# Optimization experiments

Measured on AMD Instinct MI355X. Metric: run time of the kernel, lower is better.

Reference implementation:

```python
import jax, jax.numpy as jnp
import numpy as np

B, L, DN, DE, DD, H = 2, 512, 512, 128, 128, 8
DK, DEH, DDH = DN // H, DE // H, DD // H
F = 2 * DK + DEH + 2 * DDH  # per-head concat feature size (176)
SLOPE = 0.2


def _kaiming(key, out_f, in_f):
    bound = np.sqrt(6.0 / ((1.0 + SLOPE ** 2) * in_f))
    return jax.random.uniform(key, (out_f, in_f), minval=-bound, maxval=bound, dtype=jnp.float32)


def lin(x, w, b):
    y = jnp.einsum('...i,oi->...o', x, w)
    return y if b is None else y + b


def setup_inputs() -> dict:
    key = jax.random.key(0)
    ks = jax.random.split(key, 16)
    inp = {
        'node_representation': jax.random.normal(ks[0], (B, L, DN), dtype=jnp.float32),
        'edge_representation': jax.random.normal(ks[1], (B, L, L, DE), dtype=jnp.float32),
        'diff_vec': jax.random.normal(ks[2], (B, L, DD), dtype=jnp.float32),
        'Wn_w': _kaiming(ks[3], DN, DN), 'Wn_b': jnp.zeros((DN,), jnp.float32),
        'We_w': _kaiming(ks[4], DE, DE), 'We_b': jnp.zeros((DE,), jnp.float32),
        'Wd_w': _kaiming(ks[5], DD, DD), 'Wd_b': jnp.zeros((DD,), jnp.float32),
        'Wh_w': _kaiming(ks[6], DK, DK), 'Wh_b': jnp.zeros((DK,), jnp.float32),
        'attn_w': _kaiming(ks[7], 1, F),
        'outn_w': _kaiming(ks[8], DN, DN), 'outn_b': jnp.zeros((DN,), jnp.float32),
        'Wn2_w': _kaiming(ks[9], DN, DN), 'Wn2_b': jnp.zeros((DN,), jnp.float32),
        'We2_w': _kaiming(ks[10], DE, DE), 'We2_b': jnp.zeros((DE,), jnp.float32),
        'Wd2_w': _kaiming(ks[11], DD, DD), 'Wd2_b': jnp.zeros((DD,), jnp.float32),
        'edge_w': _kaiming(ks[12], DEH, F), 'edge_b': jnp.zeros((DEH,), jnp.float32),
        'oute_w': _kaiming(ks[13], DE, DE), 'oute_b': jnp.zeros((DE,), jnp.float32),
    }
    return inp


def reference(node_representation, edge_representation, diff_vec,
              Wn_w, Wn_b, We_w, We_b, Wd_w, Wd_b, Wh_w, Wh_b, attn_w,
              outn_w, outn_b, Wn2_w, Wn2_b, We2_w, We2_b, Wd2_w, Wd2_b,
              edge_w, edge_b, oute_w, oute_b):
    lrelu = lambda x: jax.nn.leaky_relu(x, SLOPE)

    # ---- node update (GAT-style with concat score decomposed per term) ----
    npj = lin(node_representation, Wn_w, Wn_b).reshape(B, L, H, DK)
    epj = lin(edge_representation, We_w, We_b).reshape(B, L, L, H, DEH)
    dpj = lin(diff_vec, Wd_w, Wd_b).reshape(B, L, H, DDH)
    a = attn_w[0]  # concat order: [hi, hj, edge, di, dj]
    a_hi, a_hj = a[:DK], a[DK:2 * DK]
    a_e = a[2 * DK:2 * DK + DEH]
    a_di, a_dj = a[2 * DK + DEH:2 * DK + DEH + DDH], a[-DDH:]
    # scores[b,i,j,h]
    s = (jnp.einsum('blhd,d->blh', npj, a_hi)[:, :, None, :]
         + jnp.einsum('blhd,d->blh', npj, a_hj)[:, None, :, :]
         + jnp.einsum('blmhe,e->blmh', epj, a_e)
         + jnp.einsum('blhd,d->blh', dpj, a_di)[:, :, None, :]
         + jnp.einsum('blhd,d->blh', dpj, a_dj)[:, None, :, :])
    diag = jnp.eye(L, dtype=bool)[None, :, :, None]
    s = jnp.where(diag, -jnp.inf, s)
    probs = jax.nn.softmax(lrelu(s), axis=2)  # softmax over j
    node_wh = lin(npj, Wh_w, Wh_b)  # [B,L,H,DK]
    agg = jnp.einsum('blmh,bmhd->blhd', probs, node_wh)
    new_node = (npj + lrelu(agg)).reshape(B, L, DN)
    new_node = lin(new_node, outn_w, outn_b)

    # ---- edge update (concat-linear decomposed into per-term matmuls) ----
    np2 = lin(new_node, Wn2_w, Wn2_b).reshape(B, L, H, DK)
    ep2 = lin(edge_representation, We2_w, We2_b).reshape(B, L, L, H, DEH)
    dp2 = lin(diff_vec, Wd2_w, Wd2_b).reshape(B, L, H, DDH)
    # edge concat order: [edge, hi, hj, di, dj]
    W_e = edge_w[:, :DEH]
    W_hi = edge_w[:, DEH:DEH + DK]
    W_hj = edge_w[:, DEH + DK:DEH + 2 * DK]
    W_di = edge_w[:, DEH + 2 * DK:DEH + 2 * DK + DDH]
    W_dj = edge_w[:, -DDH:]
    e_out = (jnp.einsum('blmhe,fe->blmhf', ep2, W_e)
             + jnp.einsum('blhd,fd->blhf', np2, W_hi)[:, :, None]
             + jnp.einsum('blhd,fd->blhf', np2, W_hj)[:, None]
             + jnp.einsum('blhd,fd->blhf', dp2, W_di)[:, :, None]
             + jnp.einsum('blhd,fd->blhf', dp2, W_dj)[:, None]
             + edge_b)
    new_edge = lin(e_out.reshape(B, L, L, DE), oute_w, oute_b)
    return new_node, new_edge
```

## Files before the change

### kernel.cpp

```cpp
#include <hip/hip_runtime.h>
#include <hip/hip_bf16.h>

typedef unsigned short u16;
typedef unsigned short u16x8 __attribute__((ext_vector_type(8)));
typedef __bf16 bf16x8 __attribute__((ext_vector_type(8)));
typedef float f32x4 __attribute__((ext_vector_type(4)));

#define LRS 0.2f

__device__ __forceinline__ u16 f2b(float f) {
  __hip_bfloat16 h = __float2bfloat16(f);
  return __builtin_bit_cast(u16, h);
}

template<int K, int O, int KSEG, int R>
__device__ __forceinline__ void gemm_rowsR(const float* xr, const float* W, const float* bias,
                                           float* yl, float* yg, int ygstride) {
  constexpr int KPT = K / KSEG;
  constexpr int OPP = 256 / KSEG;
  const int t = threadIdx.x;
  const int ks = t % KSEG;
  const int oi = t / KSEG;
#pragma unroll
  for (int pass = 0; pass < O / OPP; ++pass) {
    const int o = pass * OPP + oi;
    float a[R];
#pragma unroll
    for (int r = 0; r < R; ++r) a[r] = 0.0f;
    const float* wp = W + (size_t)o * K + ks * KPT;
    const float* xb = xr + ks * KPT;
#pragma unroll 4
    for (int kc = 0; kc < KPT; kc += 4) {
      f32x4 w4 = *(const f32x4*)(wp + kc);
#pragma unroll
      for (int r = 0; r < R; ++r) {
        f32x4 x = *(const f32x4*)(xb + r * K + kc);
#pragma unroll
        for (int j = 0; j < 4; ++j) a[r] += x[j] * w4[j];
      }
    }
#pragma unroll
    for (int d = 1; d < KSEG; d <<= 1)
#pragma unroll
      for (int r = 0; r < R; ++r) a[r] += __shfl_xor(a[r], d, 64);
    if (ks == 0) {
      float bv = bias ? bias[o] : 0.0f;
#pragma unroll
      for (int r = 0; r < R; ++r) {
        float v = a[r] + bv;
        if (yl) yl[r * O + o] = v;
        if (yg) yg[(size_t)r * ygstride + o] = v;
      }
    }
  }
}

__global__ __launch_bounds__(256) void kW1(const float* We_w, const float* We_b, const float* attn,
                                           const float* We2_w, const float* We2_b,
                                           const float* edge_w, const float* edge_b,
                                           float* Mfull, u16* vb, float* cbe, float* sconst) {
  int gid = blockIdx.x * 256 + threadIdx.x;
  if (gid < 16384) {
    int hf = gid >> 7, c = gid & 127;
    int h = hf >> 4, fo = hf & 15;
    float s = 0;
    for (int e = 0; e < 16; ++e)
      s += edge_w[fo * 176 + e] * We2_w[(h * 16 + e) * 128 + c];
    Mfull[hf * 128 + c] = s;
  } else if (gid < 16384 + 2048) {
    int idx = gid - 16384;
    int c = idx >> 4, hc = idx & 15;
    float s = 0;
    if (hc < 8)
      for (int e = 0; e < 16; ++e)
        s += We_w[(hc * 16 + e) * 128 + c] * attn[128 + e];
    vb[c * 16 + hc] = f2b(s);
  } else if (gid < 18432 + 128) {
    int hf = gid - 18432;
    int h = hf >> 4, fo = hf & 15;
    float s = edge_b[fo];
    for (int e = 0; e < 16; ++e)
      s += We2_b[h * 16 + e] * edge_w[fo * 176 + e];
    cbe[hf] = s;
  } else if (gid < 18560 + 8) {
    int h = gid - 18560;
    float s = 0;
    for (int e = 0; e < 16; ++e)
      s += We_b[h * 16 + e] * attn[128 + e];
    sconst[h] = s;
  }
}

__global__ __launch_bounds__(256) void kW2(const float* oute_w, const float* Mfull, u16* Gb) {
  int gid = blockIdx.x * 256 + threadIdx.x;
  int o = gid >> 7, c = gid & 127;
  float s = 0;
  for (int k = 0; k < 128; ++k)
    s += oute_w[o * 128 + k] * Mfull[k * 128 + c];
  Gb[o * 128 + c] = f2b(s);
}

__global__ __launch_bounds__(256) void kN1(const float* node, const float* diff,
                                           const float* Wn_w, const float* Wn_b,
                                           const float* Wd_w, const float* Wd_b,
                                           const float* Wh_w, const float* Wh_b,
                                           const float* attn, const float* sconst,
                                           float* npj_g, float* nwh_g,
                                           float* srow_g, float* scol_g) {
  __shared__ float nrow[2 * 512], npjl[2 * 512], drow[2 * 128], dpjl[2 * 128];
  const int t = threadIdx.x;
  const int r0 = blockIdx.x * 2;
  *(f32x4*)&nrow[t * 4] = *(const f32x4*)(node + (size_t)r0 * 512 + t * 4);
  if (t < 64) *(f32x4*)&drow[t * 4] = *(const f32x4*)(diff + (size_t)r0 * 128 + t * 4);
  __syncthreads();
  gemm_rowsR<512, 512, 4, 2>(nrow, Wn_w, Wn_b, npjl, npj_g + (size_t)r0 * 512, 512);
  gemm_rowsR<128, 128, 4, 2>(drow, Wd_w, Wd_b, dpjl, nullptr, 0);
  __syncthreads();
  {
    int d = t & 63, hh = t >> 6;
#pragma unroll
    for (int hi = 0; hi < 2; ++hi) {
      int h = hh + hi * 4;
      float wb = Wh_b[d];
      float acc[2] = {wb, wb};
      for (int k = 0; k < 64; ++k) {
        float w = Wh_w[d * 64 + k];
#pragma unroll
        for (int r = 0; r < 2; ++r) acc[r] += npjl[r * 512 + h * 64 + k] * w;
      }
#pragma unroll
      for (int r = 0; r < 2; ++r) nwh_g[(size_t)(r0 + r) * 512 + h * 64 + d] = acc[r];
    }
  }
  if (t < 16) {
    int r = t >> 3, h = t & 7;
    float shi = 0, shj = 0, sdi = 0, sdj = 0;
    for (int d = 0; d < 64; ++d) {
      float x = npjl[r * 512 + h * 64 + d];
      shi += x * attn[d];
      shj += x * attn[64 + d];
    }
    for (int e = 0; e < 16; ++e) {
      float x = dpjl[r * 128 + h * 16 + e];
      sdi += x * attn[144 + e];
      sdj += x * attn[160 + e];
    }
    srow_g[(r0 + r) * 8 + h] = shi + sdi + sconst[h];
    scol_g[(r0 + r) * 8 + h] = shj + sdj;
  }
}

__global__ __launch_bounds__(256) void kA(const float* edge, const float* srow, const float* scol,
                                          const u16* vb, u16* P, float* invs, u16* abf) {
  __shared__ u16 At[2][8192];
  __shared__ float smx[512 * 9];
  __shared__ float red[256];
  __shared__ float mxh8[8];
  const int bl = blockIdx.x;
  const int b = bl >> 9, l = bl & 511;
  const int t = threadIdx.x;
  const int lane = t & 63, w = t >> 6;
  const int colL = lane & 15, kg = lane >> 4;
  const int h = t & 7, seg = t >> 3;

  bf16x8 bfr[4];
#pragma unroll
  for (int ks = 0; ks < 4; ++ks) {
    u16x8 u;
#pragma unroll
    for (int j = 0; j < 8; ++j) u[j] = vb[(ks * 32 + kg * 8 + j) * 16 + colL];
    bfr[ks] = __builtin_bit_cast(bf16x8, u);
  }

  const float* eb = edge + (size_t)bl * 65536;
  f32x4 va[8], vn[8];
#pragma unroll
  for (int j = 0; j < 4; ++j) {
    va[2 * j]     = *(const f32x4*)(eb + j * 2048 + t * 8);
    va[2 * j + 1] = *(const f32x4*)(eb + j * 2048 + t * 8 + 4);
  }
  for (int tl = 0; tl < 8; ++tl) {
    u16* cdst = abf ? abf + ((size_t)bl * 8 + tl) * 8192 : nullptr;
    u16* lbuf = At[tl & 1];
#pragma unroll
    for (int j = 0; j < 4; ++j) {
      u16x8 a8;
#pragma unroll
      for (int q = 0; q < 4; ++q) { a8[q] = f2b(va[2 * j][q]); a8[4 + q] = f2b(va[2 * j + 1][q]); }
      int c = j * 256 + t;
      int row = c >> 4, cu = c & 15;
      *(u16x8*)(lbuf + (row * 16 + (cu ^ (row & 7))) * 8) = a8;
      if (cdst) *(u16x8*)(cdst + c * 8) = a8;
    }
    if (tl < 7) {
      const float* nb2 = eb + (tl + 1) * 8192;
#pragma unroll
      for (int j = 0; j < 4; ++j) {
        vn[2 * j]     = *(const f32x4*)(nb2 + j * 2048 + t * 8);
        vn[2 * j + 1] = *(const f32x4*)(nb2 + j * 2048 + t * 8 + 4);
      }
    }
    __syncthreads();
    f32x4 acc = {0, 0, 0, 0};
#pragma unroll
    for (int ks = 0; ks < 4; ++ks) {
      int cu = ks * 4 + kg;
      int lrow = w * 16 + colL;
      bf16x8 af = *(bf16x8*)(lbuf + (lrow * 16 + (cu ^ (lrow & 7))) * 8);
      acc = __builtin_amdgcn_mfma_f32_16x16x32_bf16(af, bfr[ks], acc, 0, 0, 0);
    }
    if (colL < 8) {
#pragma unroll
      for (int r = 0; r < 4; ++r)
        smx[(tl * 64 + w * 16 + kg * 4 + r) * 9 + colL] = acc[r];
    }
#pragma unroll
    for (int q = 0; q < 8; ++q) va[q] = vn[q];
  }
  __syncthreads();

  const float srh2 = srow[(size_t)bl * 8 + h];
  float mx = -__builtin_inff();
#pragma unroll 4
  for (int i = 0; i < 16; ++i) {
    int m = seg * 16 + i;
    float sv = smx[m * 9 + h] + srh2 + scol[((size_t)b * 512 + m) * 8 + h];
    sv = (m == l) ? -__builtin_inff() : (sv >= 0.0f ? sv : LRS * sv);
    smx[m * 9 + h] = sv;
    mx = fmaxf(mx, sv);
  }
  red[t] = mx;
  __syncthreads();
  if (t < 8) {
    float m2 = -__builtin_inff();
    for (int sg = 0; sg < 32; ++sg) m2 = fmaxf(m2, red[sg * 8 + t]);
    mxh8[t] = m2;
  }
  __syncthreads();
  float mh = mxh8[h];
  float smv = 0;
#pragma unroll 4
  for (int i = 0; i < 16; ++i) {
    int m = seg * 16 + i;
    float p = __expf(smx[m * 9 + h] - mh);
    smx[m * 9 + h] = p;
    smv += p;
  }
  red[t] = smv;
  __syncthreads();
  if (t < 8) {
    float s2 = 0;
    for (int sg = 0; sg < 32; ++sg) s2 += red[sg * 8 + t];
    invs[(size_t)bl * 8 + t] = 1.0f / s2;
  }
  __syncthreads();
#pragma unroll
  for (int k = 0; k < 2; ++k) {
    int c = k * 256 + t;
    int hp = c >> 6, mb = (c & 63) * 8;
    u16x8 pk;
#pragma unroll
    for (int j = 0; j < 8; ++j) pk[j] = f2b(smx[(mb + j) * 9 + hp]);
    *(u16x8*)(P + (((size_t)b * 8 + hp) * 512 + l) * 512 + mb) = pk;
  }
}

__global__ __launch_bounds__(256) void kAgg(const u16* P, const float* nwh, const float* npj,
                                            const float* invs, float* nnp) {
  __shared__ u16 Pt[8192];
  __shared__ u16 Vt[8192];
  const int bid = blockIdx.x;
  const int lt = bid & 7, h = (bid >> 3) & 7, b = bid >> 6;
  const int l0 = lt * 64;
  const int t = threadIdx.x;
  const int lane = t & 63, w = t >> 6;
  const int colL = lane & 15, kg = lane >> 4;

  f32x4 acc[4] = {};
  for (int mc = 0; mc < 4; ++mc) {
#pragma unroll
    for (int q = 0; q < 4; ++q) {
      int c = q * 256 + t;
      int row = c >> 4, cu = c & 15;
      u16x8 a8 = *(const u16x8*)(P + (((size_t)b * 8 + h) * 512 + l0 + row) * 512 + mc * 128 + cu * 8);
      *(u16x8*)(Pt + (row * 16 + (cu ^ (row & 7))) * 8) = a8;
    }
#pragma unroll
    for (int q = 0; q < 8; ++q) {
      int c = q * 256 + t;
      int m = c >> 4, d4 = (c & 15) * 4;
      f32x4 v = *(const f32x4*)(nwh + ((size_t)b * 512 + mc * 128 + m) * 512 + h * 64 + d4);
#pragma unroll
      for (int j = 0; j < 4; ++j) {
        int d = d4 + j;
        Vt[(d * 16 + ((m >> 3) ^ (d & 7))) * 8 + (m & 7)] = f2b(v[j]);
      }
    }
    __syncthreads();
#pragma unroll
    for (int kc = 0; kc < 4; ++kc) {
      int cu = kc * 4 + kg;
      int prow = w * 16 + colL;
      bf16x8 af = *(bf16x8*)(Pt + (prow * 16 + (cu ^ (prow & 7))) * 8);
#pragma unroll
      for (int n = 0; n < 4; ++n) {
        int d = n * 16 + colL;
        bf16x8 bf = *(bf16x8*)(Vt + (d * 16 + (cu ^ (d & 7))) * 8);
        acc[n] = __builtin_amdgcn_mfma_f32_16x16x32_bf16(af, bf, acc[n], 0, 0, 0);
      }
    }
    __syncthreads();
  }
#pragma unroll
  for (int r = 0; r < 4; ++r) {
    int l = l0 + w * 16 + kg * 4 + r;
    float iv = invs[((size_t)b * 512 + l) * 8 + h];
#pragma unroll
    for (int n = 0; n < 4; ++n) {
      int o = h * 64 + n * 16 + colL;
      size_t idx = ((size_t)b * 512 + l) * 512 + o;
      float a = acc[n][r] * iv;
      a = a >= 0.0f ? a : LRS * a;
      nnp[idx] = npj[idx] + a;
    }
  }
}

__global__ __launch_bounds__(256) void kN234(const float* nnp, const float* diff,
                                             const float* outn_w, const float* outn_b,
                                             const float* Wn2_w, const float* Wn2_b,
                                             const float* Wd2_w, const float* Wd2_b,
                                             const float* edge_w, const float* cbe,
                                             const float* oute_w, const float* oute_b,
                                             float* out0, float* Pl, float* Pm) {
  __shared__ float xr[2 * 512], o0l[2 * 512], np2l[2 * 512], dr[2 * 128], dp2l[2 * 128];
  __shared__ float Rls[2 * 128], Rms[2 * 128];
  const int t = threadIdx.x;
  const int r0 = blockIdx.x * 2;
  *(f32x4*)&xr[t * 4] = *(const f32x4*)(nnp + (size_t)r0 * 512 + t * 4);
  if (t < 64) *(f32x4*)&dr[t * 4] = *(const f32x4*)(diff + (size_t)r0 * 128 + t * 4);
  __syncthreads();
  gemm_rowsR<512, 512, 4, 2>(xr, outn_w, outn_b, o0l, out0 + (size_t)r0 * 512, 512);
  gemm_rowsR<128, 128, 4, 2>(dr, Wd2_w, Wd2_b, dp2l, nullptr, 0);
  __syncthreads();
  gemm_rowsR<512, 512, 4, 2>(o0l, Wn2_w, Wn2_b, np2l, nullptr, 0);
  __syncthreads();
  {
    int hf = t & 127, which = t >> 7;
    int h = hf >> 4, fo = hf & 15;
    const float* wh = edge_w + fo * 176 + 16 + which * 64;
    const float* wd = edge_w + fo * 176 + 144 + which * 16;
    float add = which ? 0.0f : cbe[hf];
    float* dst = which ? Rms : Rls;
#pragma unroll
    for (int r = 0; r < 2; ++r) {
      float a = add;
      for (int d = 0; d < 64; ++d) a += np2l[r * 512 + h * 64 + d] * wh[d];
      for (int e = 0; e < 16; ++e) a += dp2l[r * 128 + h * 16 + e] * wd[e];
      dst[r * 128 + hf] = a;
    }
  }
  __syncthreads();
  gemm_rowsR<128, 128, 4, 2>(Rls, oute_w, oute_b, nullptr, Pl + (size_t)r0 * 128, 128);
  gemm_rowsR<128, 128, 4, 2>(Rms, oute_w, nullptr, nullptr, Pm + (size_t)r0 * 128, 128);
}

__global__ __launch_bounds__(256) void kEc(const u16* Abf, const u16* Gb,
                                           const float* Pl, const float* Pm, float* oute) {
  __shared__ u16 Gt[16384];
  __shared__ u16 At[8192];
  const int tile = blockIdx.x;
  const int bl = tile >> 2;
  const int b = bl >> 9;
  const int q0 = (tile & 3) * 128;
  const int t = threadIdx.x, lane = t & 63, w = t >> 6;
#pragma unroll
  for (int i2 = 0; i2 < 8; ++i2) {
    int u = i2 * 256 + t;
    int row = u >> 4, cu = u & 15;
    *(u16x8*)(Gt + (row * 16 + (cu ^ (row & 7))) * 8) = *(const u16x8*)(Gb + u * 8);
  }
  const int wr = w >> 1, wc = w & 1;
  const int colL = lane & 15, kg = lane >> 4;
  const float* plp = Pl + (size_t)bl * 128;
  f32x4 plv4[4];
#pragma unroll
  for (int n = 0; n < 4; ++n) plv4[n] = *(const f32x4*)(plp + wc * 64 + n * 16 + kg * 4);

  for (int sub = 0; sub < 2; ++sub) {
    const int r0 = q0 + sub * 64;
    const int gs = (tile & 3) * 2 + sub;
    const u16* src = Abf + ((size_t)bl * 8 + gs) * 8192;
#pragma unroll
    for (int q = 0; q < 4; ++q) {
      int c = q * 256 + t;
      u16x8 a8 = *(const u16x8*)(src + c * 8);
      int row = c >> 4, cu = c & 15;
      *(u16x8*)(At + (row * 16 + (cu ^ (row & 7))) * 8) = a8;
    }
    __syncthreads();
    f32x4 acc[2][4] = {};
#pragma unroll
    for (int ks = 0; ks < 4; ++ks) {
      int cu = ks * 4 + kg;
      bf16x8 af[2], bfv[4];
#pragma unroll
      for (int i = 0; i < 2; ++i) {
        int row = wr * 32 + i * 16 + colL;
        af[i] = *(bf16x8*)(At + (row * 16 + (cu ^ (row & 7))) * 8);
      }
#pragma unroll
      for (int n = 0; n < 4; ++n) {
        int orow = wc * 64 + n * 16 + colL;
        bfv[n] = *(bf16x8*)(Gt + (orow * 16 + (cu ^ (orow & 7))) * 8);
      }
#pragma unroll
      for (int i = 0; i < 2; ++i)
#pragma unroll
        for (int n = 0; n < 4; ++n)
          acc[i][n] = __builtin_amdgcn_mfma_f32_16x16x32_bf16(bfv[n], af[i], acc[i][n], 0, 0, 0);
    }
    float* ob = oute + ((size_t)bl * 512 + r0) * 128;
#pragma unroll
    for (int i = 0; i < 2; ++i) {
      int m = wr * 32 + i * 16 + colL;
      const float* pmp = Pm + ((size_t)b * 512 + r0 + m) * 128;
      float* orow = ob + (size_t)m * 128;
#pragma unroll
      for (int n = 0; n < 4; ++n) {
        int oc = wc * 64 + n * 16 + kg * 4;
        f32x4 pm4 = *(const f32x4*)(pmp + oc);
        f32x4 o4;
#pragma unroll
        for (int r = 0; r < 4; ++r) o4[r] = acc[i][n][r] + plv4[n][r] + pm4[r];
        *(f32x4*)(orow + oc) = o4;
      }
    }
    __syncthreads();
  }
}

__global__ __launch_bounds__(256) void kEd(const float* edge, const u16* Gb,
                                           const float* Pl, const float* Pm, float* oute) {
  __shared__ u16 Gt[16384];
  __shared__ u16 At[8192];
  const int tile = blockIdx.x;
  const int bl = tile >> 2;
  const int b = bl >> 9;
  const int q0 = (tile & 3) * 128;
  const int t = threadIdx.x, lane = t & 63, w = t >> 6;
#pragma unroll
  for (int i2 = 0; i2 < 8; ++i2) {
    int u = i2 * 256 + t;
    int row = u >> 4, cu = u & 15;
    *(u16x8*)(Gt + (row * 16 + (cu ^ (row & 7))) * 8) = *(const u16x8*)(Gb + u * 8);
  }
  const int wr = w >> 1, wc = w & 1;
  const int colL = lane & 15, kg = lane >> 4;
  const float* plp = Pl + (size_t)bl * 128;
  f32x4 plv4[4];
#pragma unroll
  for (int n = 0; n < 4; ++n) plv4[n] = *(const f32x4*)(plp + wc * 64 + n * 16 + kg * 4);
  const int arow = t >> 2, aseg = t & 3;

  for (int sub = 0; sub < 2; ++sub) {
    const int r0 = q0 + sub * 64;
    {
      const float* p = edge + ((size_t)bl * 512 + r0 + arow) * 128 + aseg * 32;
      f32x4 v[8];
#pragma unroll
      for (int q = 0; q < 8; ++q) v[q] = *(const f32x4*)(p + q * 4);
#pragma unroll
      for (int jj = 0; jj < 4; ++jj) {
        u16x8 a8;
#pragma unroll
        for (int j2 = 0; j2 < 4; ++j2) {
          a8[j2]     = f2b(v[2 * jj][j2]);
          a8[4 + j2] = f2b(v[2 * jj + 1][j2]);
        }
        int cu = aseg * 4 + jj;
        *(u16x8*)(At + (arow * 16 + (cu ^ (arow & 7))) * 8) = a8;
      }
    }
    __syncthreads();
    f32x4 acc[2][4] = {};
#pragma unroll
    for (int ks = 0; ks < 4; ++ks) {
      int cu = ks * 4 + kg;
      bf16x8 af[2], bfv[4];
#pragma unroll
      for (int i = 0; i < 2; ++i) {
        int row = wr * 32 + i * 16 + colL;
        af[i] = *(bf16x8*)(At + (row * 16 + (cu ^ (row & 7))) * 8);
      }
#pragma unroll
      for (int n = 0; n < 4; ++n) {
        int orow = wc * 64 + n * 16 + colL;
        bfv[n] = *(bf16x8*)(Gt + (orow * 16 + (cu ^ (orow & 7))) * 8);
      }
#pragma unroll
      for (int i = 0; i < 2; ++i)
#pragma unroll
        for (int n = 0; n < 4; ++n)
          acc[i][n] = __builtin_amdgcn_mfma_f32_16x16x32_bf16(bfv[n], af[i], acc[i][n], 0, 0, 0);
    }
    float* ob = oute + ((size_t)bl * 512 + r0) * 128;
#pragma unroll
    for (int i = 0; i < 2; ++i) {
      int m = wr * 32 + i * 16 + colL;
      const float* pmp = Pm + ((size_t)b * 512 + r0 + m) * 128;
      float* orow = ob + (size_t)m * 128;
#pragma unroll
      for (int n = 0; n < 4; ++n) {
        int oc = wc * 64 + n * 16 + kg * 4;
        f32x4 pm4 = *(const f32x4*)(pmp + oc);
        f32x4 o4;
#pragma unroll
        for (int r = 0; r < 4; ++r) o4[r] = acc[i][n][r] + plv4[n][r] + pm4[r];
        *(f32x4*)(orow + oc) = o4;
      }
    }
    __syncthreads();
  }
}

extern "C" void kernel_launch(void* const* d_in, const int* in_sizes, int n_in,
                              void* d_out, int out_size, void* d_ws, size_t ws_size,
                              hipStream_t stream) {
  (void)in_sizes; (void)n_in; (void)out_size;
  const float* node   = (const float*)d_in[0];
  const float* edge   = (const float*)d_in[1];
  const float* diff   = (const float*)d_in[2];
  const float* Wn_w   = (const float*)d_in[3];
  const float* Wn_b   = (const float*)d_in[4];
  const float* We_w   = (const float*)d_in[5];
  const float* We_b   = (const float*)d_in[6];
  const float* Wd_w   = (const float*)d_in[7];
  const float* Wd_b   = (const float*)d_in[8];
  const float* Wh_w   = (const float*)d_in[9];
  const float* Wh_b   = (const float*)d_in[10];
  const float* attn   = (const float*)d_in[11];
  const float* outn_w = (const float*)d_in[12];
  const float* outn_b = (const float*)d_in[13];
  const float* Wn2_w  = (const float*)d_in[14];
  const float* Wn2_b  = (const float*)d_in[15];
  const float* We2_w  = (const float*)d_in[16];
  const float* We2_b  = (const float*)d_in[17];
  const float* Wd2_w  = (const float*)d_in[18];
  const float* Wd2_b  = (const float*)d_in[19];
  const float* edge_w = (const float*)d_in[20];
  const float* edge_b = (const float*)d_in[21];
  const float* oute_w = (const float*)d_in[22];
  const float* oute_b = (const float*)d_in[23];

  float* out0 = (float*)d_out;
  float* out1 = out0 + 524288;

  float* f = (float*)d_ws;
  size_t off = 0;
  auto alloc = [&](size_t n) { float* p = f + off; off += (n + 7) & ~(size_t)7; return p; };
  float* npj    = alloc(524288);
  float* nwh    = alloc(524288);
  float* srow   = alloc(8192);
  float* scol   = alloc(8192);
  float* sconst = alloc(8);
  float* cbe    = alloc(128);
  float* Mfull  = alloc(16384);
  float* nnp    = alloc(524288);
  float* Pl     = alloc(131072);
  float* Pm     = alloc(131072);
  float* invs   = alloc(8192);
  u16* vb = (u16*)(f + off); off += 1024;
  u16* Gb = (u16*)(f + off); off += 8192;
  u16* P  = (u16*)(f + off); off += 2097152;
  const size_t abf_elems = (size_t)2 * 512 * 512 * 128;
  bool cache = ws_size >= off * 4 + abf_elems * 2 + 256;
  u16* Abf = cache ? (u16*)(f + off) : nullptr;

  hipLaunchKernelGGL(kW1, dim3(73), dim3(256), 0, stream,
                     We_w, We_b, attn, We2_w, We2_b, edge_w, edge_b, Mfull, vb, cbe, sconst);
  hipLaunchKernelGGL(kW2, dim3(64), dim3(256), 0, stream, oute_w, Mfull, Gb);
  hipLaunchKernelGGL(kN1, dim3(512), dim3(256), 0, stream,
                     node, diff, Wn_w, Wn_b, Wd_w, Wd_b, Wh_w, Wh_b, attn, sconst,
                     npj, nwh, srow, scol);
  hipLaunchKernelGGL(kA, dim3(1024), dim3(256), 0, stream,
                     edge, srow, scol, vb, P, invs, Abf);
  hipLaunchKernelGGL(kAgg, dim3(128), dim3(256), 0, stream, P, nwh, npj, invs, nnp);
  hipLaunchKernelGGL(kN234, dim3(512), dim3(256), 0, stream,
                     nnp, diff, outn_w, outn_b, Wn2_w, Wn2_b, Wd2_w, Wd2_b,
                     edge_w, cbe, oute_w, oute_b, out0, Pl, Pm);
  if (cache)
    hipLaunchKernelGGL(kEc, dim3(4096), dim3(256), 0, stream, Abf, Gb, Pl, Pm, out1);
  else
    hipLaunchKernelGGL(kEd, dim3(4096), dim3(256), 0, stream, edge, Gb, Pl, Pm, out1);
}
```

Measured before the change: 460.1 us.

## Feed MFMA from registers in kA and shrink edge-output tiles with register-held weights

kA no longer stages each edge tile through a double-buffered LDS array with block barriers. Each wave now loads its own rows from global memory, converts them to bf16 and passes them straight to MFMA, while still writing the cached bf16 copy in row-major order. kEc/kEd now handle 64 rows per block over twice as many blocks, with each wave keeping its slice of the G weight in registers instead of copying the whole matrix to LDS. This removes barriers and LDS traffic and frees LDS for occupancy, at the cost of less latency hiding in kA, which no longer prefetches, and redundant G loads per block.

```diff
diff --git a/kernel.cpp b/kernel.cpp
--- a/kernel.cpp
+++ b/kernel.cpp
@@ -152,7 +152,6 @@
 
 __global__ __launch_bounds__(256) void kA(const float* edge, const float* srow, const float* scol,
                                           const u16* vb, u16* P, float* invs, u16* abf) {
-  __shared__ u16 At[2][8192];
   __shared__ float smx[512 * 9];
   __shared__ float red[256];
   __shared__ float mxh8[8];
@@ -173,49 +172,28 @@
   }
 
   const float* eb = edge + (size_t)bl * 65536;
-  f32x4 va[8], vn[8];
-#pragma unroll
-  for (int j = 0; j < 4; ++j) {
-    va[2 * j]     = *(const f32x4*)(eb + j * 2048 + t * 8);
-    va[2 * j + 1] = *(const f32x4*)(eb + j * 2048 + t * 8 + 4);
-  }
-  for (int tl = 0; tl < 8; ++tl) {
-    u16* cdst = abf ? abf + ((size_t)bl * 8 + tl) * 8192 : nullptr;
-    u16* lbuf = At[tl & 1];
-#pragma unroll
-    for (int j = 0; j < 4; ++j) {
+  u16* cb = abf ? abf + (size_t)bl * 65536 : nullptr;
+
+  for (int ci = 0; ci < 8; ++ci) {
+    const int r0 = w * 128 + ci * 16;
+    const int row = r0 + colL;
+    const float* rp = eb + (size_t)row * 128;
+    f32x4 acc = {0, 0, 0, 0};
+#pragma unroll
+    for (int ks = 0; ks < 4; ++ks) {
+      f32x4 e0 = *(const f32x4*)(rp + ks * 32 + kg * 8);
+      f32x4 e1 = *(const f32x4*)(rp + ks * 32 + kg * 8 + 4);
       u16x8 a8;
 #pragma unroll
-      for (int q = 0; q < 4; ++q) { a8[q] = f2b(va[2 * j][q]); a8[4 + q] = f2b(va[2 * j + 1][q]); }
-      int c = j * 256 + t;
-      int row = c >> 4, cu = c & 15;
-      *(u16x8*)(lbuf + (row * 16 + (cu ^ (row & 7))) * 8) = a8;
-      if (cdst) *(u16x8*)(cdst + c * 8) = a8;
-    }
-    if (tl < 7) {
-      const float* nb2 = eb + (tl + 1) * 8192;
-#pragma unroll
-      for (int j = 0; j < 4; ++j) {
-        vn[2 * j]     = *(const f32x4*)(nb2 + j * 2048 + t * 8);
-        vn[2 * j + 1] = *(const f32x4*)(nb2 + j * 2048 + t * 8 + 4);
-      }
-    }
-    __syncthreads();
-    f32x4 acc = {0, 0, 0, 0};
-#pragma unroll
-    for (int ks = 0; ks < 4; ++ks) {
-      int cu = ks * 4 + kg;
-      int lrow = w * 16 + colL;
-      bf16x8 af = *(bf16x8*)(lbuf + (lrow * 16 + (cu ^ (lrow & 7))) * 8);
-      acc = __builtin_amdgcn_mfma_f32_16x16x32_bf16(af, bfr[ks], acc, 0, 0, 0);
+      for (int j = 0; j < 4; ++j) { a8[j] = f2b(e0[j]); a8[4 + j] = f2b(e1[j]); }
+      if (cb) *(u16x8*)(cb + (size_t)row * 128 + ks * 32 + kg * 8) = a8;
+      acc = __builtin_amdgcn_mfma_f32_16x16x32_bf16(__builtin_bit_cast(bf16x8, a8), bfr[ks], acc, 0, 0, 0);
     }
     if (colL < 8) {
 #pragma unroll
       for (int r = 0; r < 4; ++r)
-        smx[(tl * 64 + w * 16 + kg * 4 + r) * 9 + colL] = acc[r];
-    }
-#pragma unroll
-    for (int q = 0; q < 8; ++q) va[q] = vn[q];
+        smx[(r0 + kg * 4 + r) * 9 + colL] = acc[r];
+    }
   }
   __syncthreads();
 
@@ -367,160 +345,136 @@
 
 __global__ __launch_bounds__(256) void kEc(const u16* Abf, const u16* Gb,
                                            const float* Pl, const float* Pm, float* oute) {
-  __shared__ u16 Gt[16384];
   __shared__ u16 At[8192];
   const int tile = blockIdx.x;
-  const int bl = tile >> 2;
+  const int bl = tile >> 3;
   const int b = bl >> 9;
-  const int q0 = (tile & 3) * 128;
+  const int r0 = (tile & 7) * 64;
   const int t = threadIdx.x, lane = t & 63, w = t >> 6;
-#pragma unroll
-  for (int i2 = 0; i2 < 8; ++i2) {
-    int u = i2 * 256 + t;
-    int row = u >> 4, cu = u & 15;
-    *(u16x8*)(Gt + (row * 16 + (cu ^ (row & 7))) * 8) = *(const u16x8*)(Gb + u * 8);
-  }
-  const int wr = w >> 1, wc = w & 1;
   const int colL = lane & 15, kg = lane >> 4;
-  const float* plp = Pl + (size_t)bl * 128;
-  f32x4 plv4[4];
-#pragma unroll
-  for (int n = 0; n < 4; ++n) plv4[n] = *(const f32x4*)(plp + wc * 64 + n * 16 + kg * 4);
-
-  for (int sub = 0; sub < 2; ++sub) {
-    const int r0 = q0 + sub * 64;
-    const int gs = (tile & 3) * 2 + sub;
-    const u16* src = Abf + ((size_t)bl * 8 + gs) * 8192;
-#pragma unroll
-    for (int q = 0; q < 4; ++q) {
-      int c = q * 256 + t;
-      u16x8 a8 = *(const u16x8*)(src + c * 8);
-      int row = c >> 4, cu = c & 15;
-      *(u16x8*)(At + (row * 16 + (cu ^ (row & 7))) * 8) = a8;
-    }
-    __syncthreads();
-    f32x4 acc[2][4] = {};
+
+  bf16x8 gf[2][4];
+#pragma unroll
+  for (int n = 0; n < 2; ++n)
+#pragma unroll
+    for (int ks = 0; ks < 4; ++ks) {
+      int o = w * 32 + n * 16 + colL;
+      gf[n][ks] = *(const bf16x8*)(Gb + o * 128 + ks * 32 + kg * 8);
+    }
+  f32x4 plv4[2];
+#pragma unroll
+  for (int n = 0; n < 2; ++n)
+    plv4[n] = *(const f32x4*)(Pl + (size_t)bl * 128 + w * 32 + n * 16 + kg * 4);
+
+  const u16* src = Abf + ((size_t)bl * 512 + r0) * 128;
+#pragma unroll
+  for (int q = 0; q < 4; ++q) {
+    int c = q * 256 + t;
+    int row = c >> 4, cu = c & 15;
+    *(u16x8*)(At + (row * 16 + (cu ^ (row & 7))) * 8) = *(const u16x8*)(src + c * 8);
+  }
+  __syncthreads();
+
+  f32x4 acc[4][2] = {};
+#pragma unroll
+  for (int i = 0; i < 4; ++i) {
 #pragma unroll
     for (int ks = 0; ks < 4; ++ks) {
       int cu = ks * 4 + kg;
-      bf16x8 af[2], bfv[4];
-#pragma unroll
-      for (int i = 0; i < 2; ++i) {
-        int row = wr * 32 + i * 16 + colL;
-        af[i] = *(bf16x8*)(At + (row * 16 + (cu ^ (row & 7))) * 8);
-      }
-#pragma unroll
-      for (int n = 0; n < 4; ++n) {
-        int orow = wc * 64 + n * 16 + colL;
-        bfv[n] = *(bf16x8*)(Gt + (orow * 16 + (cu ^ (orow & 7))) * 8);
-      }
-#pragma unroll
-      for (int i = 0; i < 2; ++i)
-#pragma unroll
-        for (int n = 0; n < 4; ++n)
-          acc[i][n] = __builtin_amdgcn_mfma_f32_16x16x32_bf16(bfv[n], af[i], acc[i][n], 0, 0, 0);
-    }
-    float* ob = oute + ((size_t)bl * 512 + r0) * 128;
-#pragma unroll
-    for (int i = 0; i < 2; ++i) {
-      int m = wr * 32 + i * 16 + colL;
-      const float* pmp = Pm + ((size_t)b * 512 + r0 + m) * 128;
-      float* orow = ob + (size_t)m * 128;
-#pragma unroll
-      for (int n = 0; n < 4; ++n) {
-        int oc = wc * 64 + n * 16 + kg * 4;
-        f32x4 pm4 = *(const f32x4*)(pmp + oc);
-        f32x4 o4;
-#pragma unroll
-        for (int r = 0; r < 4; ++r) o4[r] = acc[i][n][r] + plv4[n][r] + pm4[r];
-        *(f32x4*)(orow + oc) = o4;
-      }
-    }
-    __syncthreads();
+      int row = i * 16 + colL;
+      bf16x8 af = *(bf16x8*)(At + (row * 16 + (cu ^ (row & 7))) * 8);
+#pragma unroll
+      for (int n = 0; n < 2; ++n)
+        acc[i][n] = __builtin_amdgcn_mfma_f32_16x16x32_bf16(gf[n][ks], af, acc[i][n], 0, 0, 0);
+    }
+  }
+  float* ob = oute + ((size_t)bl * 512 + r0) * 128;
+#pragma unroll
+  for (int i = 0; i < 4; ++i) {
+    int m = i * 16 + colL;
+    const float* pmp = Pm + ((size_t)b * 512 + r0 + m) * 128;
+    float* orow = ob + (size_t)m * 128;
+#pragma unroll
+    for (int n = 0; n < 2; ++n) {
+      int oc = w * 32 + n * 16 + kg * 4;
+      f32x4 pm4 = *(const f32x4*)(pmp + oc);
+      f32x4 o4;
+#pragma unroll
+      for (int r = 0; r < 4; ++r) o4[r] = acc[i][n][r] + plv4[n][r] + pm4[r];
+      *(f32x4*)(orow + oc) = o4;
+    }
   }
 }
 
 __global__ __launch_bounds__(256) void kEd(const float* edge, const u16* Gb,
                                            const float* Pl, const float* Pm, float* oute) {
-  __shared__ u16 Gt[16384];
   __shared__ u16 At[8192];
   const int tile = blockIdx.x;
-  const int bl = tile >> 2;
+  const int bl = tile >> 3;
   const int b = bl >> 9;
-  const int q0 = (tile & 3) * 128;
+  const int r0 = (tile & 7) * 64;
   const int t = threadIdx.x, lane = t & 63, w = t >> 6;
-#pragma unroll
-  for (int i2 = 0; i2 < 8; ++i2) {
-    int u = i2 * 256 + t;
-    int row = u >> 4, cu = u & 15;
-    *(u16x8*)(Gt + (row * 16 + (cu ^ (row & 7))) * 8) = *(const u16x8*)(Gb + u * 8);
-  }
-  const int wr = w >> 1, wc = w & 1;
   const int colL = lane & 15, kg = lane >> 4;
-  const float* plp = Pl + (size_t)bl * 128;
-  f32x4 plv4[4];
-#pragma unroll
-  for (int n = 0; n < 4; ++n) plv4[n] = *(const f32x4*)(plp + wc * 64 + n * 16 + kg * 4);
+  bf16x8 gf[2][4];
+#pragma unroll
+  for (int n = 0; n < 2; ++n)
+#pragma unroll
+    for (int ks = 0; ks < 4; ++ks) {
+      int o = w * 32 + n * 16 + colL;
+      gf[n][ks] = *(const bf16x8*)(Gb + o * 128 + ks * 32 + kg * 8);
+    }
+  f32x4 plv4[2];
+#pragma unroll
+  for (int n = 0; n < 2; ++n)
+    plv4[n] = *(const f32x4*)(Pl + (size_t)bl * 128 + w * 32 + n * 16 + kg * 4);
+
   const int arow = t >> 2, aseg = t & 3;
-
-  for (int sub = 0; sub < 2; ++sub) {
-    const int r0 = q0 + sub * 64;
-    {
-      const float* p = edge + ((size_t)bl * 512 + r0 + arow) * 128 + aseg * 32;
-      f32x4 v[8];
-#pragma unroll
-      for (int q = 0; q < 8; ++q) v[q] = *(const f32x4*)(p + q * 4);
-#pragma unroll
-      for (int jj = 0; jj < 4; ++jj) {
-        u16x8 a8;
-#pragma unroll
-        for (int j2 = 0; j2 < 4; ++j2) {
-          a8[j2]     = f2b(v[2 * jj][j2]);
-          a8[4 + j2] = f2b(v[2 * jj + 1][j2]);
-        }
-        int cu = aseg * 4 + jj;
-        *(u16x8*)(At + (arow * 16 + (cu ^ (arow & 7))) * 8) = a8;
+  {
+    const float* p = edge + ((size_t)bl * 512 + r0 + arow) * 128 + aseg * 32;
+    f32x4 v[8];
+#pragma unroll
+    for (int q = 0; q < 8; ++q) v[q] = *(const f32x4*)(p + q * 4);
+#pragma unroll
+    for (int jj = 0; jj < 4; ++jj) {
+      u16x8 a8;
+#pragma unroll
+      for (int j2 = 0; j2 < 4; ++j2) {
+        a8[j2]     = f2b(v[2 * jj][j2]);
+        a8[4 + j2] = f2b(v[2 * jj + 1][j2]);
       }
-    }
-    __syncthreads();
-    f32x4 acc[2][4] = {};
+      int cu = aseg * 4 + jj;
+      *(u16x8*)(At + (arow * 16 + (cu ^ (arow & 7))) * 8) = a8;
+    }
+  }
+  __syncthreads();
+  f32x4 acc[4][2] = {};
+#pragma unroll
+  for (int i = 0; i < 4; ++i) {
 #pragma unroll
     for (int ks = 0; ks < 4; ++ks) {
       int cu = ks * 4 + kg;
-      bf16x8 af[2], bfv[4];
-#pragma unroll
-      for (int i = 0; i < 2; ++i) {
-        int row = wr * 32 + i * 16 + colL;
-        af[i] = *(bf16x8*)(At + (row * 16 + (cu ^ (row & 7))) * 8);
-      }
-#pragma unroll
-      for (int n = 0; n < 4; ++n) {
-        int orow = wc * 64 + n * 16 + colL;
-        bfv[n] = *(bf16x8*)(Gt + (orow * 16 + (cu ^ (orow & 7))) * 8);
-      }
-#pragma unroll
-      for (int i = 0; i < 2; ++i)
-#pragma unroll
-        for (int n = 0; n < 4; ++n)
-          acc[i][n] = __builtin_amdgcn_mfma_f32_16x16x32_bf16(bfv[n], af[i], acc[i][n], 0, 0, 0);
-    }
-    float* ob = oute + ((size_t)bl * 512 + r0) * 128;
-#pragma unroll
-    for (int i = 0; i < 2; ++i) {
-      int m = wr * 32 + i * 16 + colL;
-      const float* pmp = Pm + ((size_t)b * 512 + r0 + m) * 128;
-      float* orow = ob + (size_t)m * 128;
-#pragma unroll
-      for (int n = 0; n < 4; ++n) {
-        int oc = wc * 64 + n * 16 + kg * 4;
-        f32x4 pm4 = *(const f32x4*)(pmp + oc);
-        f32x4 o4;
-#pragma unroll
-        for (int r = 0; r < 4; ++r) o4[r] = acc[i][n][r] + plv4[n][r] + pm4[r];
-        *(f32x4*)(orow + oc) = o4;
-      }
-    }
-    __syncthreads();
+      int row = i * 16 + colL;
+      bf16x8 af = *(bf16x8*)(At + (row * 16 + (cu ^ (row & 7))) * 8);
+#pragma unroll
+      for (int n = 0; n < 2; ++n)
+        acc[i][n] = __builtin_amdgcn_mfma_f32_16x16x32_bf16(gf[n][ks], af, acc[i][n], 0, 0, 0);
+    }
+  }
+  float* ob = oute + ((size_t)bl * 512 + r0) * 128;
+#pragma unroll
+  for (int i = 0; i < 4; ++i) {
+    int m = i * 16 + colL;
+    const float* pmp = Pm + ((size_t)b * 512 + r0 + m) * 128;
+    float* orow = ob + (size_t)m * 128;
+#pragma unroll
+    for (int n = 0; n < 2; ++n) {
+      int oc = w * 32 + n * 16 + kg * 4;
+      f32x4 pm4 = *(const f32x4*)(pmp + oc);
+      f32x4 o4;
+#pragma unroll
+      for (int r = 0; r < 4; ++r) o4[r] = acc[i][n][r] + plv4[n][r] + pm4[r];
+      *(f32x4*)(orow + oc) = o4;
+    }
   }
 }
 
@@ -590,7 +544,7 @@
                      nnp, diff, outn_w, outn_b, Wn2_w, Wn2_b, Wd2_w, Wd2_b,
                      edge_w, cbe, oute_w, oute_b, out0, Pl, Pm);
   if (cache)
-    hipLaunchKernelGGL(kEc, dim3(4096), dim3(256), 0, stream, Abf, Gb, Pl, Pm, out1);
+    hipLaunchKernelGGL(kEc, dim3(8192), dim3(256), 0, stream, Abf, Gb, Pl, Pm, out1);
   else
-    hipLaunchKernelGGL(kEd, dim3(4096), dim3(256), 0, stream, edge, Gb, Pl, Pm, out1);
-}
+    hipLaunchKernelGGL(kEd, dim3(8192), dim3(256), 0, stream, edge, Gb, Pl, Pm, out1);
+}
```

Result: slower. 523.0 us (+13.7%).
